# Optimization experiments

Hardware: AMD Instinct MI355X
Metric: run time of the kernel (lower is better)

## Reference

```python
import jax, jax.numpy as jnp
import numpy as np

PATCH_SIZE = 16
STRIDE = 16


def setup_inputs() -> dict:
    key = jax.random.key(0)
    k1, k2 = jax.random.split(key)
    x = jax.random.normal(k1, (64, 64, 8192), dtype=jnp.float32)
    mask = jax.random.randint(k2, (64, 8192), 0, 2, dtype=jnp.int32)
    return {"x": x, "mask": mask}


def reference(x, mask):
    B, C, S = x.shape
    P, St = PATCH_SIZE, STRIDE
    n_patches = 1 + (S - P) // St
    # window gather indices: [n_patches, P]
    idx = jnp.arange(n_patches)[:, None] * St + jnp.arange(P)[None, :]
    # x[:, :, idx] -> [B, C, n_patches, P]; torch stacks on dim=1 -> [B, n_patches, C, P]
    patches = jnp.transpose(x[:, :, idx], (0, 2, 1, 3)).reshape(B, n_patches, C * P)
    # per-patch valid ratio over the window, thresholded at 0.5 -> float mask [B, n_patches]
    valid_ratio = jnp.mean(mask[:, idx].astype(jnp.float32), axis=-1)
    padding_mask = (valid_ratio >= 0.5).astype(jnp.float32)
    return patches, padding_mask
```

## Files before the change

### kernel.cpp

```cpp
#include <hip/hip_runtime.h>


typedef float f4 __attribute__((ext_vector_type(4)));

constexpr int Bb  = 64;
constexpr int Cc  = 64;
constexpr int Ss  = 8192;
constexpr int NP  = 512;
constexpr int PT  = 16;
constexpr size_t PATCH_ELEMS = (size_t)Bb * NP * Cc * 16;

__global__ __launch_bounds__(512) void ts_patcher_kernel(
    const float* __restrict__ x,
    const int*   __restrict__ mask,
    float*       __restrict__ out)
{
    __shared__ f4 lds[Cc * 64];

    const int t   = threadIdx.x;
    const int blk = blockIdx.x;
    const int b   = blk >> 5;
    const int P0  = (blk & 31) * PT;

    const float* xb = x + (size_t)b * Cc * Ss + (size_t)P0 * 16;

    {
        const int w = t >> 6;
        const int l = t & 63;
#pragma unroll
        for (int i = 0; i < 8; ++i) {
            const int c = i * 8 + w;
            const f4 v = *(const f4*)(xb + (size_t)c * Ss + l * 4);
            lds[c * 64 + (l ^ (c & 7))] = v;
        }
    }

    __syncthreads();

    {
        float* otile = out + ((size_t)(b * NP + P0) * (Cc * 16));
        const int pl = t >> 8;
        const int tt = t & 255;
        const int c  = tt >> 2;
        const int jj = tt & 3;
#pragma unroll
        for (int i = 0; i < 8; ++i) {
            const int p = i * 2 + pl;
            const f4 v = lds[c * 64 + ((p * 4 + jj) ^ (c & 7))];
            *(f4*)(otile + (size_t)p * 1024 + (size_t)tt * 4) = v;
        }
    }

    if (t < PT) {
        const int p = P0 + t;
        const int4* m = (const int4*)(mask + (size_t)b * Ss + (size_t)p * 16);
        int4 a = m[0], d = m[1], e = m[2], f = m[3];
        int s = a.x + a.y + a.z + a.w
              + d.x + d.y + d.z + d.w
              + e.x + e.y + e.z + e.w
              + f.x + f.y + f.z + f.w;
        out[PATCH_ELEMS + (size_t)b * NP + p] = (s >= 8) ? 1.0f : 0.0f;
    }
}

extern "C" void kernel_launch(void* const* d_in, const int* in_sizes, int n_in,
                              void* d_out, int out_size, void* d_ws, size_t ws_size,
                              hipStream_t stream) {
    const float* x    = (const float*)d_in[0];
    const int*   mask = (const int*)d_in[1];
    float*       out  = (float*)d_out;

    const int blocks = Bb * (NP / PT);
    ts_patcher_kernel<<<blocks, 512, 0, stream>>>(x, mask, out);
}
```

Before: 233.0 us.

## Double-buffer LDS tiles with async global_load_lds in persistent per-block loop

Each block now handles 64 patches as 8 tiles of 8 patches each, double-buffered in LDS. Tiles are staged with the direct global-to-LDS load builtin, and manual vmcnt waits plus barriers let the next tile's loads overlap the current tile's stores. This targets load/store serialization and register staging in a memory-bound transpose. In exchange the grid shrinks to 512 blocks, which may underfill the GPU, and the hand-tuned vmcnt counts are fragile.

```diff
diff --git a/kernel.cpp b/kernel.cpp
--- a/kernel.cpp
+++ b/kernel.cpp
@@ -7,7 +7,8 @@
 constexpr int Cc  = 64;
 constexpr int Ss  = 8192;
 constexpr int NP  = 512;
-constexpr int PT  = 16;
+constexpr int PT  = 8;
+constexpr int T   = 8;
 constexpr size_t PATCH_ELEMS = (size_t)Bb * NP * Cc * 16;
 
 __global__ __launch_bounds__(512) void ts_patcher_kernel(
@@ -15,43 +16,64 @@
     const int*   __restrict__ mask,
     float*       __restrict__ out)
 {
-    __shared__ f4 lds[Cc * 64];
+    __shared__ f4 lds[2 * Cc * 32];
 
     const int t   = threadIdx.x;
+    const int w   = t >> 6;
+    const int l   = t & 63;
     const int blk = blockIdx.x;
-    const int b   = blk >> 5;
-    const int P0  = (blk & 31) * PT;
+    const int b   = blk >> 3;
+    const int P0  = (blk & 7) * (PT * T);
 
     const float* xb = x + (size_t)b * Cc * Ss + (size_t)P0 * 16;
 
-    {
-        const int w = t >> 6;
-        const int l = t & 63;
+    f4* bufA = lds;
+    f4* bufB = lds + Cc * 32;
+
+    auto STAGE = [&](int tile, f4* buf) {
 #pragma unroll
-        for (int i = 0; i < 8; ++i) {
-            const int c = i * 8 + w;
-            const f4 v = *(const f4*)(xb + (size_t)c * Ss + l * 4);
-            lds[c * 64 + (l ^ (c & 7))] = v;
+        for (int i = 0; i < 4; ++i) {
+            const int c = 16 * i + 2 * w + (l >> 5);
+            const int g = (l & 31) ^ (c & 7);
+            const float* src = xb + (size_t)tile * (PT * 16)
+                                  + (size_t)c * Ss + (size_t)g * 4;
+            __builtin_amdgcn_global_load_lds(
+                (const __attribute__((address_space(1))) void*)src,
+                (__attribute__((address_space(3))) void*)&buf[(16 * i + 2 * w) * 32],
+                16, 0, 0);
         }
+    };
+
+    STAGE(0, bufA);
+    STAGE(1, bufB);
+
+    f4* ob = (f4*)(out + (size_t)(b * NP + P0) * (Cc * 16));
+
+#pragma unroll
+    for (int tile = 0; tile < T; ++tile) {
+        if (tile == 0 || tile == T - 1) {
+            asm volatile("s_waitcnt vmcnt(4)" ::: "memory");
+        } else {
+            asm volatile("s_waitcnt vmcnt(8)" ::: "memory");
+        }
+        __builtin_amdgcn_s_barrier();
+
+        f4* buf = (tile & 1) ? bufB : bufA;
+        f4* ot  = ob + (size_t)tile * (PT * 256);
+#pragma unroll
+        for (int j = 0; j < 4; ++j) {
+            const int o  = (j * 8 + w) * 64 + l;
+            const int p  = o >> 8;
+            const int r  = o & 255;
+            const int c  = r >> 2;
+            const int jj = r & 3;
+            ot[o] = buf[c * 32 + ((4 * p + jj) ^ (c & 7))];
+        }
+        __builtin_amdgcn_s_barrier();
+        if (tile + 2 < T) STAGE(tile + 2, buf);
     }
 
-    __syncthreads();
-
-    {
-        float* otile = out + ((size_t)(b * NP + P0) * (Cc * 16));
-        const int pl = t >> 8;
-        const int tt = t & 255;
-        const int c  = tt >> 2;
-        const int jj = tt & 3;
-#pragma unroll
-        for (int i = 0; i < 8; ++i) {
-            const int p = i * 2 + pl;
-            const f4 v = lds[c * 64 + ((p * 4 + jj) ^ (c & 7))];
-            *(f4*)(otile + (size_t)p * 1024 + (size_t)tt * 4) = v;
-        }
-    }
-
-    if (t < PT) {
+    if (t < PT * T) {
         const int p = P0 + t;
         const int4* m = (const int4*)(mask + (size_t)b * Ss + (size_t)p * 16);
         int4 a = m[0], d = m[1], e = m[2], f = m[3];
@@ -70,6 +92,6 @@
     const int*   mask = (const int*)d_in[1];
     float*       out  = (float*)d_out;
 
-    const int blocks = Bb * (NP / PT);
+    const int blocks = Bb * (NP / (PT * T));
     ts_patcher_kernel<<<blocks, 512, 0, stream>>>(x, mask, out);
 }
```

Result: slower. 239.4 us (+2.8%).
